# Optimization experiments

Measured on AMD Instinct MI355X. Metric: run time of the kernel, lower is better.

## Reference

```python
import jax, jax.numpy as jnp
import numpy as np

B, T, E, H, P = 512, 512, 64, 128, 96


def setup_inputs() -> dict:
    key = jax.random.key(0)
    ks = jax.random.split(key, 12)
    s = 1.0 / np.sqrt(H)  # torch GRU/Linear uniform init scale
    u = lambda k, shape: jax.random.uniform(k, shape, jnp.float32, -s, s)
    return {
        "x": jax.random.normal(ks[0], (B, T, E), jnp.float32),
        "W_ih0": u(ks[1], (3 * H, E)),
        "W_hh0": u(ks[2], (3 * H, H)),
        "b_ih0": u(ks[3], (3 * H,)),
        "b_hh0": u(ks[4], (3 * H,)),
        "W_ih1": u(ks[5], (3 * H, H)),
        "W_hh1": u(ks[6], (3 * H, H)),
        "b_ih1": u(ks[7], (3 * H,)),
        "b_hh1": u(ks[8], (3 * H,)),
        "W_head": u(ks[9], (P, H)),
        "b_head": u(ks[10], (P,)),
    }


def _gru_layer(x, W_ih, W_hh, b_ih, b_hh):
    # x: [B, T, F]; PyTorch gate order: r, z, n
    Bn, Tn, _ = x.shape
    Hn = W_hh.shape[1]
    # precompute input-side gates for all timesteps: [B, T, 3H]
    xg = jnp.einsum('btf,gf->btg', x, W_ih) + b_ih

    def step(h, xg_t):
        hg = h @ W_hh.T + b_hh                      # [B, 3H]
        xr, xz, xn = jnp.split(xg_t, 3, axis=-1)
        hr, hz, hn = jnp.split(hg, 3, axis=-1)
        r = jax.nn.sigmoid(xr + hr)
        z = jax.nn.sigmoid(xz + hz)
        n = jnp.tanh(xn + r * hn)
        h_new = (1.0 - z) * n + z * h
        return h_new, h_new

    h0 = jnp.zeros((Bn, Hn), x.dtype)
    _, ys = jax.lax.scan(step, h0, jnp.swapaxes(xg, 0, 1))  # ys: [T, B, H]
    return jnp.swapaxes(ys, 0, 1)                            # [B, T, H]


def reference(x, W_ih0, W_hh0, b_ih0, b_hh0, W_ih1, W_hh1, b_ih1, b_hh1, W_head, b_head):
    h1 = _gru_layer(x, W_ih0, W_hh0, b_ih0, b_hh0)
    h2 = _gru_layer(h1, W_ih1, W_hh1, b_ih1, b_hh1)
    last = h2[:, -1, :]                   # [B, H]
    return last @ W_head.T + b_head       # [B, pred_len]
```

## Files before the change

### kernel.cpp

```cpp
#include <hip/hip_runtime.h>


#define B_SZ 512
#define T_SZ 512
#define E_SZ 64
#define H_SZ 128
#define P_SZ 96
#define NB   16
#define NGRP (B_SZ / NB)
#define SC_SIG  (-1.44269504f)
#define SC_TANH (-2.88539008f)

typedef _Float16 half8 __attribute__((ext_vector_type(8)));
typedef float    f32x4 __attribute__((ext_vector_type(4)));

__device__ __forceinline__ float exp2_(float x) {
#if __has_builtin(__builtin_amdgcn_exp2f)
    return __builtin_amdgcn_exp2f(x);
#else
    return exp2f(x);
#endif
}
__device__ __forceinline__ float rcp_(float x) {
#if __has_builtin(__builtin_amdgcn_rcpf)
    return __builtin_amdgcn_rcpf(x);
#else
    return 1.0f / x;
#endif
}

__device__ __forceinline__ int swz256(int row, int byte) {
    return row * 256 + (byte ^ ((row & 7) << 4));
}

__device__ __forceinline__ void load_bfrag(const float* __restrict__ W, int ldk,
                                           int n0, int kt, int ln, float scale,
                                           half8* hi) {
    int n = n0 + (ln & 15);
    int k = kt * 32 + (ln >> 4) * 8;
    const float* p = W + (size_t)n * ldk + k;
    float4 a = *(const float4*)p;
    float4 b = *(const float4*)(p + 4);
    float v[8] = {a.x, a.y, a.z, a.w, b.x, b.y, b.z, b.w};
    half8 h;
    #pragma unroll
    for (int j = 0; j < 8; ++j)
        h[j] = (_Float16)(v[j] * scale);
    *hi = h;
}

#define LOADX(Sx, tt)                                                              \
    if ((tt) < T_SZ) {                                                             \
        _Pragma("unroll") for (int kt = 0; kt < KFX; ++kt)                         \
            Sx[kt] = *(const half8*)(xlane + (size_t)(tt) * ROWB + kt * 64);       \
    }

#define GRU_STEP(Sx, tcur, tnext)                                                  \
    {                                                                              \
        const char* hb = hs[(tcur) & 1];                                           \
        half8 ah[4];                                                               \
        _Pragma("unroll") for (int kt = 0; kt < 4; ++kt)                           \
            ah[kt] = *(const half8*)(hb + swz256(colg, kt * 64 + rgrp * 16));      \
        f32x4 ax0 = {bs0, bs0, bs0, bs0};                                          \
        f32x4 ax1 = {bs1, bs1, bs1, bs1};                                          \
        f32x4 ax2 = {bi2s, bi2s, bi2s, bi2s};                                      \
        f32x4 cNH = {bh2s, bh2s, bh2s, bh2s};                                      \
        _Pragma("unroll") for (int kt = 0; kt < KFX; ++kt) {                       \
            ax0 = __builtin_amdgcn_mfma_f32_16x16x32_f16(Sx[kt], bx[0][kt], ax0, 0, 0, 0); \
            ax1 = __builtin_amdgcn_mfma_f32_16x16x32_f16(Sx[kt], bx[1][kt], ax1, 0, 0, 0); \
            ax2 = __builtin_amdgcn_mfma_f32_16x16x32_f16(Sx[kt], bx[2][kt], ax2, 0, 0, 0); \
        }                                                                          \
        __builtin_amdgcn_s_setprio(1);                                             \
        _Pragma("unroll") for (int kt = 0; kt < 4; ++kt) {                         \
            ax0 = __builtin_amdgcn_mfma_f32_16x16x32_f16(ah[kt], bhh[0][kt], ax0, 0, 0, 0); \
            ax1 = __builtin_amdgcn_mfma_f32_16x16x32_f16(ah[kt], bhh[1][kt], ax1, 0, 0, 0); \
            cNH = __builtin_amdgcn_mfma_f32_16x16x32_f16(ah[kt], bhh[2][kt], cNH, 0, 0, 0); \
        }                                                                          \
        LOADX(Sx, tnext)                                                           \
        float hn_[4];                                                              \
        _Pragma("unroll") for (int j = 0; j < 4; ++j) {                            \
            float rr = rcp_(1.f + exp2_(ax0[j]));                                  \
            float zz = rcp_(1.f + exp2_(ax1[j]));                                  \
            float v  = ax2[j] + rr * cNH[j];                                       \
            float nn = fmaf(2.f, rcp_(1.f + exp2_(v)), -1.f);                      \
            hn_[j] = nn + zz * (hreg[j] - nn);                                     \
            hreg[j] = hn_[j];                                                      \
        }                                                                          \
        __builtin_amdgcn_s_setprio(0);                                             \
        char* hw = hs[((tcur) + 1) & 1];                                           \
        _Pragma("unroll") for (int j = 0; j < 4; ++j) {                            \
            int bb = rgrp * 4 + j;                                                 \
            *(_Float16*)(hw + swz256(bb, cw * 2)) = (_Float16)hn_[j];              \
            if constexpr (OUT_ALL) {                                               \
                ((_Float16*)hout)[((size_t)(b0 + bb) * T_SZ + (tcur)) * H_SZ + cw] \
                    = (_Float16)hn_[j];                                            \
            }                                                                      \
        }                                                                          \
           \
        asm volatile("s_waitcnt lgkmcnt(0)" ::: "memory");                         \
        __builtin_amdgcn_s_barrier();                                              \
        __builtin_amdgcn_sched_barrier(0);                                         \
    }

template<int K_IN, bool OUT_ALL, int ROLE>
__device__ __forceinline__ void gru_body(const _Float16* __restrict__ xin,
                                         const float* __restrict__ W_ih,
                                         const float* __restrict__ W_hh,
                                         const float* __restrict__ b_ih,
                                         const float* __restrict__ b_hh,
                                         void* __restrict__ hout,
                                         const float* __restrict__ W_head,
                                         const float* __restrict__ b_head,
                                         float* __restrict__ out,
                                         int* __restrict__ prog,
                                         int grp, char (*hs)[4096])
{
    constexpr int KFX  = K_IN / 32;
    constexpr int ROWB = K_IN * 2;

    const int tid  = threadIdx.x;
    const int ln   = tid & 63;
    const int wv   = tid >> 6;
    const int colg = ln & 15;
    const int rgrp = ln >> 4;
    const int b0   = grp * NB;
    const int cw   = wv * 16 + colg;

    half8 bx[3][KFX];
    half8 bhh[3][4];
    const float gsc[3] = {SC_SIG, SC_SIG, SC_TANH};
    #pragma unroll
    for (int g = 0; g < 3; ++g) {
        int n0 = g * 128 + wv * 16;
        #pragma unroll
        for (int kt = 0; kt < KFX; ++kt)
            load_bfrag(W_ih, K_IN, n0, kt, ln, gsc[g], &bx[g][kt]);
        #pragma unroll
        for (int kt = 0; kt < 4; ++kt)
            load_bfrag(W_hh, H_SZ, n0, kt, ln, gsc[g], &bhh[g][kt]);
    }
    const float bs0  = SC_SIG  * (b_ih[cw] + b_hh[cw]);
    const float bs1  = SC_SIG  * (b_ih[128 + cw] + b_hh[128 + cw]);
    const float bi2s = SC_TANH * b_ih[256 + cw];
    const float bh2s = SC_TANH * b_hh[256 + cw];

    half8 bph[4];
    float bhd = 0.f;
    if (ROLE == 1 && wv < 6) {
        #pragma unroll
        for (int kt = 0; kt < 4; ++kt)
            load_bfrag(W_head, H_SZ, wv * 16, kt, ln, 1.0f, &bph[kt]);
        bhd = b_head[cw];
    }

    if (tid < 256) *(float4*)(hs[0] + tid * 16) = make_float4(0.f, 0.f, 0.f, 0.f);
    float hreg[4] = {0.f, 0.f, 0.f, 0.f};

    const char* xlane = (const char*)xin
        + (size_t)(b0 + colg) * T_SZ * ROWB
        + rgrp * 16;

    int avail = 0;
    if (ROLE == 1) {
        while (avail < 4) {
            avail = __hip_atomic_load(prog, __ATOMIC_ACQUIRE, __HIP_MEMORY_SCOPE_AGENT);
            if (avail < 4) __builtin_amdgcn_s_sleep(8);
        }
    }

    half8 Ax[KFX], Bx2[KFX];
    LOADX(Ax, 0)
    LOADX(Bx2, 1)
    __syncthreads();

    for (int t = 0; t < T_SZ; t += 2) {
        if (ROLE == 1 && avail < T_SZ) {
            const int need = (t + 4 < T_SZ) ? t + 4 : T_SZ;
            while (avail < need) {
                avail = __hip_atomic_load(prog, __ATOMIC_ACQUIRE, __HIP_MEMORY_SCOPE_AGENT);
                if (avail < need) __builtin_amdgcn_s_sleep(8);
            }
        }
        GRU_STEP(Ax,  t,     t + 2)
        GRU_STEP(Bx2, t + 1, t + 3)
        if (ROLE == 0 && (t & 7) == 6) {
            asm volatile("s_waitcnt vmcnt(0)" ::: "memory");
            __builtin_amdgcn_s_barrier();
            if (tid == 0)
                __hip_atomic_store(prog, t + 2, __ATOMIC_RELEASE, __HIP_MEMORY_SCOPE_AGENT);
        }
    }

    if (ROLE == 1 && wv < 6) {
        half8 ahf[4];
        #pragma unroll
        for (int kt = 0; kt < 4; ++kt)
            ahf[kt] = *(const half8*)(hs[0] + swz256(colg, kt * 64 + rgrp * 16));
        f32x4 acc = {bhd, bhd, bhd, bhd};
        #pragma unroll
        for (int kt = 0; kt < 4; ++kt)
            acc = __builtin_amdgcn_mfma_f32_16x16x32_f16(ahf[kt], bph[kt], acc, 0, 0, 0);
        #pragma unroll
        for (int j = 0; j < 4; ++j)
            out[(size_t)(b0 + rgrp * 4 + j) * P_SZ + cw] = acc[j];
    }
}

__global__ __launch_bounds__(512)
void gru_fused(const _Float16* __restrict__ xh,
               _Float16* __restrict__ h1,
               const float* __restrict__ W_ih0, const float* __restrict__ W_hh0,
               const float* __restrict__ b_ih0, const float* __restrict__ b_hh0,
               const float* __restrict__ W_ih1, const float* __restrict__ W_hh1,
               const float* __restrict__ b_ih1, const float* __restrict__ b_hh1,
               const float* __restrict__ W_head, const float* __restrict__ b_head,
               float* __restrict__ out,
               int* __restrict__ prog)
{
    __shared__ __align__(16) char hs[2][4096];
    const int role = blockIdx.x >> 5;
    const int grp  = blockIdx.x & 31;
    if (role == 0)
        gru_body<E_SZ, true, 0>(xh, W_ih0, W_hh0, b_ih0, b_hh0, h1,
                                W_head, b_head, out, prog + grp, grp, hs);
    else
        gru_body<H_SZ, false, 1>(h1, W_ih1, W_hh1, b_ih1, b_hh1, nullptr,
                                 W_head, b_head, out, prog + grp, grp, hs);
}

__global__ __launch_bounds__(256)
void cvt_f32_f16(const float* __restrict__ in, _Float16* __restrict__ out, int n8)
{
    int i = blockIdx.x * 256 + threadIdx.x;
    if (i >= n8) return;
    const float4* p = (const float4*)in + (size_t)i * 2;
    float4 a = p[0];
    float4 b = p[1];
    half8 h;
    h[0] = (_Float16)a.x; h[1] = (_Float16)a.y; h[2] = (_Float16)a.z; h[3] = (_Float16)a.w;
    h[4] = (_Float16)b.x; h[5] = (_Float16)b.y; h[6] = (_Float16)b.z; h[7] = (_Float16)b.w;
    ((half8*)out)[i] = h;
}

extern "C" void kernel_launch(void* const* d_in, const int* in_sizes, int n_in,
                              void* d_out, int out_size, void* d_ws, size_t ws_size,
                              hipStream_t stream)
{
    const float* x      = (const float*)d_in[0];
    const float* W_ih0  = (const float*)d_in[1];
    const float* W_hh0  = (const float*)d_in[2];
    const float* b_ih0  = (const float*)d_in[3];
    const float* b_hh0  = (const float*)d_in[4];
    const float* W_ih1  = (const float*)d_in[5];
    const float* W_hh1  = (const float*)d_in[6];
    const float* b_ih1  = (const float*)d_in[7];
    const float* b_hh1  = (const float*)d_in[8];
    const float* W_head = (const float*)d_in[9];
    const float* b_head = (const float*)d_in[10];
    float* out = (float*)d_out;

    char* ws = (char*)d_ws;
    _Float16* h1  = (_Float16*)ws;
    _Float16* xh  = (_Float16*)(ws + (64u << 20));
    int*      prg = (int*)     (ws + (96u << 20));

    hipMemsetAsync(prg, 0, NGRP * sizeof(int), stream);
    cvt_f32_f16<<<(B_SZ * T_SZ * E_SZ / 8 + 255) / 256, 256, 0, stream>>>(x, xh, B_SZ * T_SZ * E_SZ / 8);
    gru_fused<<<2 * NGRP, 512, 0, stream>>>(xh, h1,
                                            W_ih0, W_hh0, b_ih0, b_hh0,
                                            W_ih1, W_hh1, b_ih1, b_hh1,
                                            W_head, b_head, out, prg);
}
```

Baseline: 512.4 us.

## Interleave two independent batch groups per block to overlap GRU recurrence latency

Each block now runs two 16-row batch groups with separate LDS hidden-state buffers, state registers and input prefetch buffers. Their MFMA and gate phases are interleaved so one chain's work can hide the other's dependency latency, and they share one barrier per timestep. The grid shrinks from 64 to 32 blocks, the setprio hints are removed, and launch bounds now request two blocks per CU. The extra per-thread state combined with the tighter register limit from launch_bounds(512,2) risks register spills, and fewer blocks means less parallelism across CUs.

```diff
diff --git a/kernel.cpp b/kernel.cpp
--- a/kernel.cpp
+++ b/kernel.cpp
@@ -8,6 +8,7 @@
 #define P_SZ 96
 #define NB   16
 #define NGRP (B_SZ / NB)
+#define NBLK 16
 #define SC_SIG  (-1.44269504f)
 #define SC_TANH (-2.88539008f)
 
@@ -49,58 +50,61 @@
     *hi = h;
 }
 
-#define LOADX(Sx, tt)                                                              \
+#define LOADX(Sx, XL, tt)                                                          \
     if ((tt) < T_SZ) {                                                             \
         _Pragma("unroll") for (int kt = 0; kt < KFX; ++kt)                         \
-            Sx[kt] = *(const half8*)(xlane + (size_t)(tt) * ROWB + kt * 64);       \
-    }
-
-#define GRU_STEP(Sx, tcur, tnext)                                                  \
+            Sx[kt] = *(const half8*)((XL) + (size_t)(tt) * ROWB + kt * 64);        \
+    }
+
+#define GRU_MFMA(Sx, XL, HS, A0, A1, A2, CN, tcur)                                 \
     {                                                                              \
-        const char* hb = hs[(tcur) & 1];                                           \
+        const char* hb = (HS)[(tcur) & 1];                                         \
         half8 ah[4];                                                               \
         _Pragma("unroll") for (int kt = 0; kt < 4; ++kt)                           \
             ah[kt] = *(const half8*)(hb + swz256(colg, kt * 64 + rgrp * 16));      \
-        f32x4 ax0 = {bs0, bs0, bs0, bs0};                                          \
-        f32x4 ax1 = {bs1, bs1, bs1, bs1};                                          \
-        f32x4 ax2 = {bi2s, bi2s, bi2s, bi2s};                                      \
-        f32x4 cNH = {bh2s, bh2s, bh2s, bh2s};                                      \
+        A0 = (f32x4){bs0, bs0, bs0, bs0};                                          \
+        A1 = (f32x4){bs1, bs1, bs1, bs1};                                          \
+        A2 = (f32x4){bi2s, bi2s, bi2s, bi2s};                                      \
+        CN = (f32x4){bh2s, bh2s, bh2s, bh2s};                                      \
         _Pragma("unroll") for (int kt = 0; kt < KFX; ++kt) {                       \
-            ax0 = __builtin_amdgcn_mfma_f32_16x16x32_f16(Sx[kt], bx[0][kt], ax0, 0, 0, 0); \
-            ax1 = __builtin_amdgcn_mfma_f32_16x16x32_f16(Sx[kt], bx[1][kt], ax1, 0, 0, 0); \
-            ax2 = __builtin_amdgcn_mfma_f32_16x16x32_f16(Sx[kt], bx[2][kt], ax2, 0, 0, 0); \
-        }                                                                          \
-        __builtin_amdgcn_s_setprio(1);                                             \
+            A0 = __builtin_amdgcn_mfma_f32_16x16x32_f16(Sx[kt], bx[0][kt], A0, 0, 0, 0); \
+            A1 = __builtin_amdgcn_mfma_f32_16x16x32_f16(Sx[kt], bx[1][kt], A1, 0, 0, 0); \
+            A2 = __builtin_amdgcn_mfma_f32_16x16x32_f16(Sx[kt], bx[2][kt], A2, 0, 0, 0); \
+        }                                                                          \
         _Pragma("unroll") for (int kt = 0; kt < 4; ++kt) {                         \
-            ax0 = __builtin_amdgcn_mfma_f32_16x16x32_f16(ah[kt], bhh[0][kt], ax0, 0, 0, 0); \
-            ax1 = __builtin_amdgcn_mfma_f32_16x16x32_f16(ah[kt], bhh[1][kt], ax1, 0, 0, 0); \
-            cNH = __builtin_amdgcn_mfma_f32_16x16x32_f16(ah[kt], bhh[2][kt], cNH, 0, 0, 0); \
-        }                                                                          \
-        LOADX(Sx, tnext)                                                           \
+            A0 = __builtin_amdgcn_mfma_f32_16x16x32_f16(ah[kt], bhh[0][kt], A0, 0, 0, 0); \
+            A1 = __builtin_amdgcn_mfma_f32_16x16x32_f16(ah[kt], bhh[1][kt], A1, 0, 0, 0); \
+            CN = __builtin_amdgcn_mfma_f32_16x16x32_f16(ah[kt], bhh[2][kt], CN, 0, 0, 0); \
+        }                                                                          \
+        LOADX(Sx, XL, (tcur) + 2)                                                  \
+    }
+
+#define GRU_FIN(HS, HREG, A0, A1, A2, CN, BOFF, tcur)                              \
+    {                                                                              \
         float hn_[4];                                                              \
         _Pragma("unroll") for (int j = 0; j < 4; ++j) {                            \
-            float rr = rcp_(1.f + exp2_(ax0[j]));                                  \
-            float zz = rcp_(1.f + exp2_(ax1[j]));                                  \
-            float v  = ax2[j] + rr * cNH[j];                                       \
+            float rr = rcp_(1.f + exp2_(A0[j]));                                   \
+            float zz = rcp_(1.f + exp2_(A1[j]));                                   \
+            float v  = A2[j] + rr * CN[j];                                         \
             float nn = fmaf(2.f, rcp_(1.f + exp2_(v)), -1.f);                      \
-            hn_[j] = nn + zz * (hreg[j] - nn);                                     \
-            hreg[j] = hn_[j];                                                      \
-        }                                                                          \
-        __builtin_amdgcn_s_setprio(0);                                             \
-        char* hw = hs[((tcur) + 1) & 1];                                           \
+            hn_[j] = nn + zz * (HREG[j] - nn);                                     \
+            HREG[j] = hn_[j];                                                      \
+        }                                                                          \
+        char* hw = (HS)[((tcur) + 1) & 1];                                         \
         _Pragma("unroll") for (int j = 0; j < 4; ++j) {                            \
             int bb = rgrp * 4 + j;                                                 \
             *(_Float16*)(hw + swz256(bb, cw * 2)) = (_Float16)hn_[j];              \
             if constexpr (OUT_ALL) {                                               \
-                ((_Float16*)hout)[((size_t)(b0 + bb) * T_SZ + (tcur)) * H_SZ + cw] \
+                ((_Float16*)hout)[((size_t)((BOFF) + bb) * T_SZ + (tcur)) * H_SZ + cw] \
                     = (_Float16)hn_[j];                                            \
             }                                                                      \
         }                                                                          \
-           \
-        asm volatile("s_waitcnt lgkmcnt(0)" ::: "memory");                         \
-        __builtin_amdgcn_s_barrier();                                              \
-        __builtin_amdgcn_sched_barrier(0);                                         \
-    }
+    }
+
+#define HBAR                                                                       \
+    asm volatile("s_waitcnt lgkmcnt(0)" ::: "memory");                             \
+    __builtin_amdgcn_s_barrier();                                                  \
+    __builtin_amdgcn_sched_barrier(0);
 
 template<int K_IN, bool OUT_ALL, int ROLE>
 __device__ __forceinline__ void gru_body(const _Float16* __restrict__ xin,
@@ -113,7 +117,7 @@
                                          const float* __restrict__ b_head,
                                          float* __restrict__ out,
                                          int* __restrict__ prog,
-                                         int grp, char (*hs)[4096])
+                                         int gblk, char (*hsA)[4096], char (*hsB)[4096])
 {
     constexpr int KFX  = K_IN / 32;
     constexpr int ROWB = K_IN * 2;
@@ -123,7 +127,8 @@
     const int wv   = tid >> 6;
     const int colg = ln & 15;
     const int rgrp = ln >> 4;
-    const int b0   = grp * NB;
+    const int b0A  = gblk * 2 * NB;
+    const int b0B  = b0A + NB;
     const int cw   = wv * 16 + colg;
 
     half8 bx[3][KFX];
@@ -144,21 +149,17 @@
     const float bi2s = SC_TANH * b_ih[256 + cw];
     const float bh2s = SC_TANH * b_hh[256 + cw];
 
-    half8 bph[4];
-    float bhd = 0.f;
-    if (ROLE == 1 && wv < 6) {
-        #pragma unroll
-        for (int kt = 0; kt < 4; ++kt)
-            load_bfrag(W_head, H_SZ, wv * 16, kt, ln, 1.0f, &bph[kt]);
-        bhd = b_head[cw];
-    }
-
-    if (tid < 256) *(float4*)(hs[0] + tid * 16) = make_float4(0.f, 0.f, 0.f, 0.f);
-    float hreg[4] = {0.f, 0.f, 0.f, 0.f};
-
-    const char* xlane = (const char*)xin
-        + (size_t)(b0 + colg) * T_SZ * ROWB
-        + rgrp * 16;
+    if (tid < 256) {
+        *(float4*)(hsA[0] + tid * 16) = make_float4(0.f, 0.f, 0.f, 0.f);
+        *(float4*)(hsB[0] + tid * 16) = make_float4(0.f, 0.f, 0.f, 0.f);
+    }
+    float hregA[4] = {0.f, 0.f, 0.f, 0.f};
+    float hregB[4] = {0.f, 0.f, 0.f, 0.f};
+
+    const char* xlaneA = (const char*)xin
+        + (size_t)(b0A + colg) * T_SZ * ROWB + rgrp * 16;
+    const char* xlaneB = (const char*)xin
+        + (size_t)(b0B + colg) * T_SZ * ROWB + rgrp * 16;
 
     int avail = 0;
     if (ROLE == 1) {
@@ -168,9 +169,13 @@
         }
     }
 
-    half8 Ax[KFX], Bx2[KFX];
-    LOADX(Ax, 0)
-    LOADX(Bx2, 1)
+    half8 AxA[KFX], BxA[KFX], AxB[KFX], BxB[KFX];
+    LOADX(AxA, xlaneA, 0)
+    LOADX(BxA, xlaneA, 1)
+    LOADX(AxB, xlaneB, 0)
+    LOADX(BxB, xlaneB, 1)
+
+    f32x4 aA0, aA1, aA2, cA, aB0, aB1, aB2, cB;
     __syncthreads();
 
     for (int t = 0; t < T_SZ; t += 2) {
@@ -181,8 +186,16 @@
                 if (avail < need) __builtin_amdgcn_s_sleep(8);
             }
         }
-        GRU_STEP(Ax,  t,     t + 2)
-        GRU_STEP(Bx2, t + 1, t + 3)
+        GRU_MFMA(AxA, xlaneA, hsA, aA0, aA1, aA2, cA, t)
+        GRU_MFMA(AxB, xlaneB, hsB, aB0, aB1, aB2, cB, t)
+        GRU_FIN(hsA, hregA, aA0, aA1, aA2, cA, b0A, t)
+        GRU_FIN(hsB, hregB, aB0, aB1, aB2, cB, b0B, t)
+        HBAR
+        GRU_MFMA(BxA, xlaneA, hsA, aA0, aA1, aA2, cA, t + 1)
+        GRU_MFMA(BxB, xlaneB, hsB, aB0, aB1, aB2, cB, t + 1)
+        GRU_FIN(hsA, hregA, aA0, aA1, aA2, cA, b0A, t + 1)
+        GRU_FIN(hsB, hregB, aB0, aB1, aB2, cB, b0B, t + 1)
+        HBAR
         if (ROLE == 0 && (t & 7) == 6) {
             asm volatile("s_waitcnt vmcnt(0)" ::: "memory");
             __builtin_amdgcn_s_barrier();
@@ -192,21 +205,31 @@
     }
 
     if (ROLE == 1 && wv < 6) {
-        half8 ahf[4];
+        half8 bph[4];
         #pragma unroll
         for (int kt = 0; kt < 4; ++kt)
-            ahf[kt] = *(const half8*)(hs[0] + swz256(colg, kt * 64 + rgrp * 16));
-        f32x4 acc = {bhd, bhd, bhd, bhd};
-        #pragma unroll
-        for (int kt = 0; kt < 4; ++kt)
-            acc = __builtin_amdgcn_mfma_f32_16x16x32_f16(ahf[kt], bph[kt], acc, 0, 0, 0);
-        #pragma unroll
-        for (int j = 0; j < 4; ++j)
-            out[(size_t)(b0 + rgrp * 4 + j) * P_SZ + cw] = acc[j];
-    }
-}
-
-__global__ __launch_bounds__(512)
+            load_bfrag(W_head, H_SZ, wv * 16, kt, ln, 1.0f, &bph[kt]);
+        const float bhd = b_head[cw];
+        #pragma unroll
+        for (int g = 0; g < 2; ++g) {
+            const char* hsrc = g ? hsB[0] : hsA[0];
+            const int   boff = g ? b0B : b0A;
+            half8 ahf[4];
+            #pragma unroll
+            for (int kt = 0; kt < 4; ++kt)
+                ahf[kt] = *(const half8*)(hsrc + swz256(colg, kt * 64 + rgrp * 16));
+            f32x4 acc = {bhd, bhd, bhd, bhd};
+            #pragma unroll
+            for (int kt = 0; kt < 4; ++kt)
+                acc = __builtin_amdgcn_mfma_f32_16x16x32_f16(ahf[kt], bph[kt], acc, 0, 0, 0);
+            #pragma unroll
+            for (int j = 0; j < 4; ++j)
+                out[(size_t)(boff + rgrp * 4 + j) * P_SZ + cw] = acc[j];
+        }
+    }
+}
+
+__global__ __launch_bounds__(512, 2)
 void gru_fused(const _Float16* __restrict__ xh,
                _Float16* __restrict__ h1,
                const float* __restrict__ W_ih0, const float* __restrict__ W_hh0,
@@ -217,15 +240,15 @@
                float* __restrict__ out,
                int* __restrict__ prog)
 {
-    __shared__ __align__(16) char hs[2][4096];
-    const int role = blockIdx.x >> 5;
-    const int grp  = blockIdx.x & 31;
+    __shared__ __align__(16) char hs[2][2][4096];
+    const int role = blockIdx.x >> 4;
+    const int gblk = blockIdx.x & 15;
     if (role == 0)
         gru_body<E_SZ, true, 0>(xh, W_ih0, W_hh0, b_ih0, b_hh0, h1,
-                                W_head, b_head, out, prog + grp, grp, hs);
+                                W_head, b_head, out, prog + gblk, gblk, hs[0], hs[1]);
     else
         gru_body<H_SZ, false, 1>(h1, W_ih1, W_hh1, b_ih1, b_hh1, nullptr,
-                                 W_head, b_head, out, prog + grp, grp, hs);
+                                 W_head, b_head, out, prog + gblk, gblk, hs[0], hs[1]);
 }
 
 __global__ __launch_bounds__(256)
@@ -264,9 +287,9 @@
     _Float16* xh  = (_Float16*)(ws + (64u << 20));
     int*      prg = (int*)     (ws + (96u << 20));
 
-    hipMemsetAsync(prg, 0, NGRP * sizeof(int), stream);
+    hipMemsetAsync(prg, 0, NBLK * sizeof(int), stream);
     cvt_f32_f16<<<(B_SZ * T_SZ * E_SZ / 8 + 255) / 256, 256, 0, stream>>>(x, xh, B_SZ * T_SZ * E_SZ / 8);
-    gru_fused<<<2 * NGRP, 512, 0, stream>>>(xh, h1,
+    gru_fused<<<2 * NBLK, 512, 0, stream>>>(xh, h1,
                                             W_ih0, W_hh0, b_ih0, b_hh0,
                                             W_ih1, W_hh1, b_ih1, b_hh1,
                                             W_head, b_head, out, prg);
```

Result: slower. 972.2 us (+89.7%).
